# Performance work log

Measured on AMD Instinct MI355X. Metric: run time of the kernel, lower is better.

The kernel has to match this reference:

```python
import jax, jax.numpy as jnp
import numpy as np
from functools import partial

MASK_THRESH = 0.4
SCORE_THRESH = 0.35
SUPPRESS_IOU = 0.85
TOPK_KEEP = 40


def _logit(p):
    p = jnp.clip(p, 1e-4, 1.0 - 1e-4)
    return jnp.log(p) - jnp.log1p(-p)


def _greedy_keep(binm_f, labels, scores):
    # binm_f: [N, HW] float 0/1 masks, rows already sorted by descending score.
    # Precompute the pairwise mask-IoU matrix once (batched, memory-bound),
    # then run the sequential greedy suppression over the small NxN matrix.
    N = binm_f.shape[0]
    inter = binm_f @ binm_f.T                              # [N, N]
    area = jnp.sum(binm_f, axis=1)
    union = jnp.maximum(area[:, None] + area[None, :] - inter, 1.0)
    iou = inter / union
    conflict = (labels[:, None] == labels[None, :]) & (iou >= SUPPRESS_IOU)

    def body(i, state):
        kept, count, stopped = state
        stopped = stopped | (scores[i] < SCORE_THRESH)     # break on low score
        clash = jnp.any(kept & conflict[i])                # same-class high-IoU vs kept
        take = (~stopped) & (~clash)
        kept = kept.at[i].set(take)
        count = count + take.astype(jnp.int32)
        stopped = stopped | (count >= TOPK_KEEP)           # break after topk kept
        return kept, count, stopped

    kept0 = jnp.zeros((N,), dtype=bool)
    kept, count, _ = jax.lax.fori_loop(0, N, body, (kept0, jnp.int32(0), jnp.array(False)))
    return kept, count


def _per_image(masks, labels, scores, feat, class_count):
    N, H, W = masks.shape
    D, fh, fw = feat.shape
    order = jnp.argsort(-scores)
    masks = masks[order]
    labels = labels[order]
    scores = scores[order]
    binm = masks > MASK_THRESH
    kept, count = _greedy_keep(binm.reshape(N, -1).astype(masks.dtype), labels, scores)

    # pack kept entries into the leading slots, preserving score order
    key = jnp.where(kept, jnp.arange(N), N + jnp.arange(N))
    perm = jnp.argsort(key)
    masks_p = jnp.clip(masks[perm], 0.0, 1.0)
    labels_p = jnp.clip(labels[perm], 0, class_count - 1)
    scores_p = jnp.clip(scores[perm], 0.0, 1.0)
    valid = jnp.arange(N) < count                          # [Q], Q == N == max_queries

    mask_logits = jnp.where(valid[:, None, None], _logit(masks_p), -20.0)

    C1 = class_count + 1
    base = jnp.full((N, C1), -10.0, dtype=masks.dtype)     # default row (all -10)
    row = base.at[:, -1].set(0.0)                          # no-object col -> 0
    onehot = jax.nn.one_hot(labels_p, C1, dtype=masks.dtype)
    row = row + onehot * (_logit(scores_p)[:, None] + 10.0)
    class_logits = jnp.where(valid[:, None], row, base)

    binm_p = masks_p > MASK_THRESH
    xs = jnp.arange(W, dtype=masks.dtype)
    ys = jnp.arange(H, dtype=masks.dtype)
    big = jnp.asarray(1e9, masks.dtype)
    x1 = jnp.min(jnp.where(binm_p, xs[None, None, :], big), axis=(1, 2))
    x2 = jnp.max(jnp.where(binm_p, xs[None, None, :], -big), axis=(1, 2))
    y1 = jnp.min(jnp.where(binm_p, ys[None, :, None], big), axis=(1, 2))
    y2 = jnp.max(jnp.where(binm_p, ys[None, :, None], -big), axis=(1, 2))
    cx = (x1 + x2) * 0.5 / W
    cy = (y1 + y2) * 0.5 / H
    bw = jnp.maximum(x2 - x1, 0.0) / W
    bh = jnp.maximum(y2 - y1, 0.0) / H
    box = jnp.clip(jnp.stack([cx, cy, bw, bh], axis=-1), 0.0, 1.0)
    has_px = jnp.any(binm_p, axis=(1, 2))
    boxes = jnp.where((valid & has_px)[:, None], box, 0.0)

    # mask-pooled DINO embeddings (bilinear downsample == F.interpolate align_corners=False)
    mask_small = jax.image.resize(masks_p, (N, fh, fw), method='linear')
    denom = jnp.maximum(jnp.sum(mask_small, axis=(1, 2)), 1e-6)
    pooled = jnp.einsum('qhw,dhw->qd', mask_small, feat) / denom[:, None]
    norm = jnp.maximum(jnp.linalg.norm(pooled, axis=-1, keepdims=True), 1e-12)
    embs = jnp.where(valid[:, None], pooled / norm, 0.0)
    return mask_logits, class_logits, boxes, embs


def reference(masks, labels, scores, dino_feat_map, class_count):
    fn = lambda m, l, s, f: _per_image(m, l, s, f, class_count)
    return jax.vmap(fn)(masks, labels, scores, dino_feat_map)


def setup_inputs():
    key = jax.random.key(0)
    k1, k2, k3, k4 = jax.random.split(key, 4)
    B, N, H, W = 2, 100, 640, 640
    D, fh, fw = 384, 40, 40
    return {
        'masks': jax.random.uniform(k1, (B, N, H, W), dtype=jnp.float32),
        'labels': jax.random.randint(k2, (B, N), 0, 80),
        'scores': jax.random.uniform(k3, (B, N), dtype=jnp.float32),
        'dino_feat_map': jax.random.normal(k4, (B, D, fh, fw), dtype=jnp.float32),
        'class_count': 80,
    }
```

## Files before the change

### kernel.cpp

```cpp
#include <hip/hip_runtime.h>
#include <cstdint>
#include <climits>

constexpr int kB = 2;
constexpr int kN = 100;
constexpr int kH = 640;
constexpr int kW = 640;
constexpr int kHW = kH * kW;
constexpr int kWORDS = kHW / 64;
constexpr int kD = 384;
constexpr int kFH = 40;
constexpr int kFW = 40;
constexpr int kC = 80;
constexpr int kC1 = kC + 1;
constexpr int kTOPK = 40;
constexpr int kCW = 2;
constexpr int kPairMax = kN * (kN - 1) / 2;

constexpr float MASK_THRESH = 0.4f;
constexpr float SCORE_THRESH = 0.35f;
constexpr float SUPPRESS_IOU = 0.85f;

constexpr size_t O_MASK = 0;
constexpr size_t O_CLS  = (size_t)kB * kN * kHW;
constexpr size_t O_BOX  = O_CLS + (size_t)kB * kN * kC1;
constexpr size_t O_EMB  = O_BOX + (size_t)kB * kN * 4;

typedef float floatx4 __attribute__((ext_vector_type(4)));
__device__ __forceinline__ void nt_store4(const float4& v, float4* p) {
    floatx4 t; t.x = v.x; t.y = v.y; t.z = v.z; t.w = v.w;
    __builtin_nontemporal_store(t, (floatx4*)p);
}

__device__ __forceinline__ float logitf_(float p) {
    p = fminf(fmaxf(p, 1e-4f), 1.0f - 1e-4f);
    return logf(p) - log1pf(-p);
}

__device__ __forceinline__ float logit_fast(float p) {
    p = fminf(fmaxf(p, 1e-4f), 1.0f - 1e-4f);
    float r = __fdividef(p, 1.0f - p);
    return __log2f(r) * 0.69314718056f;
}

__global__ void k0_sort_init(const float* __restrict__ scores,
                             const int* __restrict__ labels,
                             int* __restrict__ order, float* __restrict__ sScore,
                             int* __restrict__ sLabel, int* __restrict__ area,
                             int* __restrict__ bbox,
                             unsigned long long* __restrict__ confRow,
                             float* __restrict__ denom,
                             int* __restrict__ pairList,
                             int* __restrict__ pairCount) {
    int b = blockIdx.x;
    int t = threadIdx.x;
    __shared__ float s[kN];
    __shared__ int   lb[kN];
    __shared__ float ssort[kN];
    __shared__ int   lsort[kN];
    if (t < kN) { s[t] = scores[b * kN + t]; lb[t] = labels[b * kN + t]; }
    if (t == 0) pairCount[b] = 0;
    __syncthreads();
    if (t < kN) {
        float si = s[t];
        int rank = 0;
        for (int j = 0; j < kN; ++j) {
            float sj = s[j];
            if (sj > si || (sj == si && j < t)) rank++;
        }
        order[b * kN + rank]  = t;
        sScore[b * kN + rank] = si;
        sLabel[b * kN + rank] = lb[t];
        ssort[rank] = si;
        lsort[rank] = lb[t];
        area[b * kN + t] = 0;
        bbox[(b * kN + t) * 4 + 0] = INT_MAX;
        bbox[(b * kN + t) * 4 + 1] = INT_MIN;
        bbox[(b * kN + t) * 4 + 2] = INT_MAX;
        bbox[(b * kN + t) * 4 + 3] = INT_MIN;
        confRow[(b * kN + t) * kCW + 0] = 0ull;
        confRow[(b * kN + t) * kCW + 1] = 0ull;
        if (t < kTOPK) denom[b * kTOPK + t] = 0.0f;
    }
    __syncthreads();
    for (int idx = t; idx < kN * kN; idx += 128) {
        int i = idx / kN, j = idx - i * kN;
        if (j < i && lsort[i] == lsort[j] && ssort[i] >= SCORE_THRESH) {
            int pos = atomicAdd(&pairCount[b], 1);
            pairList[b * kPairMax + pos] = (i << 16) | j;
        }
    }
}

constexpr int kSPLIT = 8;
__global__ __launch_bounds__(256) void k1_pack(
    const float* __restrict__ masks, const int* __restrict__ order,
    const float* __restrict__ sScore, unsigned long long* __restrict__ packed,
    int* __restrict__ area, int* __restrict__ bbox) {
    int b = blockIdx.z, slot = blockIdx.y;
    if (sScore[b * kN + slot] < SCORE_THRESH) return;
    int q = order[b * kN + slot];
    const float4* src = (const float4*)(masks + (size_t)(b * kN + q) * kHW);
    unsigned long long* dst = packed + (size_t)(b * kN + slot) * (size_t)kWORDS;
    int lane = threadIdx.x & 63;
    int wv = threadIdx.x >> 6;
    const int wordsPerBlock = kWORDS / kSPLIT;
    const int wordsPerWave = wordsPerBlock / 4;
    int wbase = blockIdx.x * wordsPerBlock + wv * wordsPerWave;
    int pixBase = wbase * 64;

    int areaAcc = 0;
    int x1 = INT_MAX, x2 = INT_MIN, y1 = INT_MAX, y2 = INT_MIN;
#pragma unroll 2
    for (int i = 0; i < wordsPerWave / 4; ++i) {
        int pix = pixBase + i * 256 + lane * 4;
        float4 v = src[pix >> 2];
        bool p0 = v.x > MASK_THRESH, p1 = v.y > MASK_THRESH;
        bool p2 = v.z > MASK_THRESH, p3 = v.w > MASK_THRESH;
        unsigned long long b0 = __ballot(p0);
        unsigned long long b1 = __ballot(p1);
        unsigned long long b2 = __ballot(p2);
        unsigned long long b3 = __ballot(p3);
        if (lane == 0) {
            dst[wbase + 4 * i + 0] = b0;
            dst[wbase + 4 * i + 1] = b1;
            dst[wbase + 4 * i + 2] = b2;
            dst[wbase + 4 * i + 3] = b3;
        }
        int cnt = (int)p0 + (int)p1 + (int)p2 + (int)p3;
        areaAcc += cnt;
        if (cnt) {
            int row  = pix / kW;
            int col0 = pix - row * kW;
            int lo = p0 ? 0 : (p1 ? 1 : (p2 ? 2 : 3));
            int hi = p3 ? 3 : (p2 ? 2 : (p1 ? 1 : 0));
            x1 = min(x1, col0 + lo); x2 = max(x2, col0 + hi);
            y1 = min(y1, row);       y2 = max(y2, row);
        }
    }
#pragma unroll
    for (int off = 32; off > 0; off >>= 1) {
        areaAcc += __shfl_down(areaAcc, off);
        x1 = min(x1, __shfl_down(x1, off));
        x2 = max(x2, __shfl_down(x2, off));
        y1 = min(y1, __shfl_down(y1, off));
        y2 = max(y2, __shfl_down(y2, off));
    }
    __shared__ int sA[4], sx1[4], sx2[4], sy1[4], sy2[4];
    if (lane == 0) { sA[wv] = areaAcc; sx1[wv] = x1; sx2[wv] = x2; sy1[wv] = y1; sy2[wv] = y2; }
    __syncthreads();
    if (threadIdx.x == 0) {
        int A   = sA[0] + sA[1] + sA[2] + sA[3];
        int bx1 = min(min(sx1[0], sx1[1]), min(sx1[2], sx1[3]));
        int bx2 = max(max(sx2[0], sx2[1]), max(sx2[2], sx2[3]));
        int by1 = min(min(sy1[0], sy1[1]), min(sy1[2], sy1[3]));
        int by2 = max(max(sy2[0], sy2[1]), max(sy2[2], sy2[3]));
        if (A) atomicAdd(&area[b * kN + slot], A);
        if (bx1 != INT_MAX) {
            atomicMin(&bbox[(b * kN + slot) * 4 + 0], bx1);
            atomicMax(&bbox[(b * kN + slot) * 4 + 1], bx2);
            atomicMin(&bbox[(b * kN + slot) * 4 + 2], by1);
            atomicMax(&bbox[(b * kN + slot) * 4 + 3], by2);
        }
    }
}

__global__ __launch_bounds__(256) void k2a_conflict(
    const unsigned long long* __restrict__ packed,
    const int* __restrict__ area, const int* __restrict__ pairList,
    const int* __restrict__ pairCount, unsigned long long* __restrict__ confRow) {
    int b = blockIdx.y;
    int np = pairCount[b];
    __shared__ int s[256];
    for (int p = blockIdx.x; p < np; p += gridDim.x) {
        int pr = pairList[b * kPairMax + p];
        int i = pr >> 16, j = pr & 0xffff;
        const unsigned long long* pi = packed + (size_t)(b * kN + i) * kWORDS;
        const unsigned long long* pj = packed + (size_t)(b * kN + j) * kWORDS;
        int acc = 0;
        for (int w = threadIdx.x; w < kWORDS; w += 256)
            acc += __popcll(pi[w] & pj[w]);
        s[threadIdx.x] = acc;
        __syncthreads();
        for (int st = 128; st > 0; st >>= 1) {
            if (threadIdx.x < st) s[threadIdx.x] += s[threadIdx.x + st];
            __syncthreads();
        }
        if (threadIdx.x == 0) {
            float inter = (float)s[0];
            float un = fmaxf((float)area[b * kN + i] + (float)area[b * kN + j] - inter, 1.0f);
            if (inter / un >= SUPPRESS_IOU)
                atomicOr(&confRow[(b * kN + i) * kCW + (j >> 6)], 1ull << (j & 63));
        }
        __syncthreads();
    }
}

__global__ __launch_bounds__(256) void k2b_greedy_clsbox(
    const float* __restrict__ sScore, const int* __restrict__ order,
    const unsigned long long* __restrict__ confRow,
    const int* __restrict__ sLabel, const int* __restrict__ area,
    const int* __restrict__ bbox, int* __restrict__ src_q,
    int* __restrict__ keep_s, int* __restrict__ countArr,
    float* __restrict__ out) {
    int b = blockIdx.x;
    int t = threadIdx.x;
    __shared__ float sc[kN];
    __shared__ int   ord[kN];
    __shared__ unsigned long long cr[kN * kCW];
    __shared__ int   ks[kN];
    __shared__ int   cnt_s;
    for (int e = t; e < kN; e += 256) {
        sc[e]  = sScore[b * kN + e];
        ord[e] = order[b * kN + e];
    }
    for (int e = t; e < kN * kCW; e += 256)
        cr[e] = confRow[(size_t)b * kN * kCW + e];
    __syncthreads();

    if (t == 0) {
        unsigned long long keptLo = 0ull, keptHi = 0ull;
        bool stopped = false;
        int count = 0;
        for (int i = 0; i < kN; ++i) {
            if (sc[i] < SCORE_THRESH) stopped = true;
            unsigned long long cl = cr[i * kCW + 0] & keptLo;
            unsigned long long ch = cr[i * kCW + 1] & keptHi;
            bool take = (!stopped) && ((cl | ch) == 0ull);
            if (take) {
                if (i < 64) keptLo |= 1ull << i; else keptHi |= 1ull << (i - 64);
                src_q[b * kN + count]  = ord[i];
                keep_s[b * kN + count] = i;
                ks[count] = i;
                count++;
                if (count >= kTOPK) stopped = true;
            }
        }
        countArr[b] = count;
        cnt_s = count;
        for (int s = count; s < kN; ++s) {
            src_q[b * kN + s] = -1; keep_s[b * kN + s] = -1; ks[s] = -1;
        }
    }
    __syncthreads();
    int count = cnt_s;

    for (int e = t; e < kN * kC1; e += 256) {
        int slot = e / kC1, c = e % kC1;
        float val = -10.0f;
        if (slot < count) {
            int s2 = ks[slot];
            int lab = min(max(sLabel[b * kN + s2], 0), kC - 1);
            float scv = fminf(fmaxf(sc[s2], 0.f), 1.f);
            if (c == lab) val = logitf_(scv);
            else if (c == kC1 - 1) val = 0.0f;
        }
        out[O_CLS + (size_t)b * kN * kC1 + e] = val;
    }
    for (int slot = t; slot < kN; slot += 256) {
        float bx[4] = {0.f, 0.f, 0.f, 0.f};
        if (slot < count) {
            int s2 = ks[slot];
            if (area[b * kN + s2] > 0) {
                float x1 = (float)bbox[(b * kN + s2) * 4 + 0];
                float x2 = (float)bbox[(b * kN + s2) * 4 + 1];
                float y1 = (float)bbox[(b * kN + s2) * 4 + 2];
                float y2 = (float)bbox[(b * kN + s2) * 4 + 3];
                bx[0] = fminf(fmaxf((x1 + x2) * 0.5f / kW, 0.f), 1.f);
                bx[1] = fminf(fmaxf((y1 + y2) * 0.5f / kH, 0.f), 1.f);
                bx[2] = fminf(fmaxf(fmaxf(x2 - x1, 0.f) / kW, 0.f), 1.f);
                bx[3] = fminf(fmaxf(fmaxf(y2 - y1, 0.f) / kH, 0.f), 1.f);
            }
        }
        for (int c4 = 0; c4 < 4; ++c4)
            out[O_BOX + (size_t)(b * kN + slot) * 4 + c4] = bx[c4];
    }
}

__global__ __launch_bounds__(256) void k3_logits_resizex(
    const float* __restrict__ masks, const int* __restrict__ src_q,
    float* __restrict__ out, float* __restrict__ S1) {
    int b = blockIdx.z, slot = blockIdx.y;
    int q = src_q[b * kN + slot];
    int lane = threadIdx.x & 63, wv = threadIdx.x >> 6;
    int y = blockIdx.x * 4 + wv;
    float4* dst = (float4*)(out + O_MASK + (size_t)(b * kN + slot) * kHW) + (size_t)y * 160;

    if (q < 0) {
        float4 f = make_float4(-20.f, -20.f, -20.f, -20.f);
        nt_store4(f, dst + lane);
        nt_store4(f, dst + 64 + lane);
        if (lane < 32) nt_store4(f, dst + 128 + lane);
        return;
    }

    __shared__ float rbuf[4][660];
    const float4* src = (const float4*)(masks + (size_t)(b * kN + q) * kHW) + (size_t)y * 160;
#pragma unroll
    for (int i = 0; i < 3; ++i) {
        int idx = i * 64 + lane;
        if (idx < 160) {
            float4 m = src[idx];
            float4 o;
            o.x = logit_fast(m.x); o.y = logit_fast(m.y);
            o.z = logit_fast(m.z); o.w = logit_fast(m.w);
            nt_store4(o, dst + idx);
            int col = idx * 4;
            int pad = col >> 5;
            rbuf[wv][col + pad + 0] = fminf(fmaxf(m.x, 0.f), 1.f);
            rbuf[wv][col + pad + 1] = fminf(fmaxf(m.y, 0.f), 1.f);
            rbuf[wv][col + pad + 2] = fminf(fmaxf(m.z, 0.f), 1.f);
            rbuf[wv][col + pad + 3] = fminf(fmaxf(m.w, 0.f), 1.f);
        }
    }
    __syncthreads();
    if (lane < kFW) {
        int ox = lane;
        float c = 16.0f * ox + 7.5f;
        float s = 0.f;
#pragma unroll
        for (int t = 0; t < 32; ++t) {
            int j = 16 * ox - 8 + t;
            if (j >= 0 && j < kW) {
                float w = 1.0f - fabsf((float)j - c) * (1.0f / 16.0f);
                s += w * rbuf[wv][j + (j >> 5)];
            }
        }
        float rs = (ox == 0 || ox == kFW - 1) ? (1.0f / 14.0f) : (1.0f / 16.0f);
        S1[((size_t)(b * kTOPK + slot) * kH + y) * kFW + ox] = s * rs;
    }
}

__global__ __launch_bounds__(256) void k3f_fill(float* __restrict__ out) {
    int b = blockIdx.y;
    float4* base = (float4*)(out + O_MASK + ((size_t)b * kN + kTOPK) * (size_t)kHW);
    const size_t n4 = (size_t)(kN - kTOPK) * kHW / 4;
    float4 f = make_float4(-20.f, -20.f, -20.f, -20.f);
    for (size_t i = (size_t)blockIdx.x * 256 + threadIdx.x; i < n4;
         i += (size_t)gridDim.x * 256)
        nt_store4(f, base + i);
}

__global__ __launch_bounds__(256) void k6_resize_y(
    const float* __restrict__ S1, const int* __restrict__ countArr,
    float* __restrict__ msmall, float* __restrict__ denom) {
    int k = blockIdx.y, b = blockIdx.z;
    if (k >= countArr[b]) return;
    const float* src = S1 + (size_t)(b * kTOPK + k) * kH * kFW;
    int e0 = blockIdx.x * 320;
    float tot = 0.f;
    for (int ee = threadIdx.x; ee < 320; ee += 256) {
        int e = e0 + ee;
        int oy = e / kFW, ox = e % kFW;
        float c = 16.0f * oy + 7.5f;
        int j0 = max(0, 16 * oy - 8), j1 = min(kH - 1, 16 * oy + 23);
        float s = 0.f;
        for (int j = j0; j <= j1; ++j) {
            float w = 1.0f - fabsf((float)j - c) * (1.0f / 16.0f);
            s += w * src[(size_t)j * kFW + ox];
        }
        float rs = (oy == 0 || oy == kFH - 1) ? (1.0f / 14.0f) : (1.0f / 16.0f);
        s *= rs;
        msmall[(size_t)(b * kTOPK + k) * kFH * kFW + e] = s;
        tot += s;
    }
    __shared__ float sm[256];
    sm[threadIdx.x] = tot;
    __syncthreads();
    for (int st = 128; st > 0; st >>= 1) {
        if (threadIdx.x < st) sm[threadIdx.x] += sm[threadIdx.x + st];
        __syncthreads();
    }
    if (threadIdx.x == 0) atomicAdd(&denom[b * kTOPK + k], sm[0]);
}

__global__ __launch_bounds__(256) void k7_pool(
    const float* __restrict__ feat, const float* __restrict__ msmall,
    const float* __restrict__ denom, const int* __restrict__ countArr,
    float* __restrict__ pooled) {
    int d = blockIdx.x, b = blockIdx.y;
    int lane = threadIdx.x & 63, wv = threadIdx.x >> 6;
    const float* fp = feat + ((size_t)b * kD + d) * (kFH * kFW);
    float f[25];
#pragma unroll
    for (int i = 0; i < 25; ++i) f[i] = fp[i * 64 + lane];
    int count = countArr[b];
    for (int k = wv; k < count; k += 4) {
        const float* sp = msmall + (size_t)(b * kTOPK + k) * (kFH * kFW);
        float acc = 0.f;
#pragma unroll
        for (int i = 0; i < 25; ++i) acc += f[i] * sp[i * 64 + lane];
        for (int off = 32; off > 0; off >>= 1) acc += __shfl_down(acc, off);
        if (lane == 0)
            pooled[(size_t)(b * kTOPK + k) * kD + d] =
                acc / fmaxf(denom[b * kTOPK + k], 1e-6f);
    }
}

__global__ void k8_embs(const float* __restrict__ pooled,
                        const int* __restrict__ countArr,
                        float* __restrict__ out) {
    int slot = blockIdx.x, b = blockIdx.y;
    int count = countArr[b];
    float* dst = out + O_EMB + (size_t)(b * kN + slot) * kD;
    if (slot >= count) {
        for (int e = threadIdx.x; e < kD; e += 128) dst[e] = 0.f;
        return;
    }
    const float* p = pooled + (size_t)(b * kTOPK + slot) * kD;
    float ss = 0.f;
    for (int e = threadIdx.x; e < kD; e += 128) { float v = p[e]; ss += v * v; }
    __shared__ float sm[128];
    sm[threadIdx.x] = ss;
    __syncthreads();
    for (int st = 64; st > 0; st >>= 1) {
        if (threadIdx.x < st) sm[threadIdx.x] += sm[threadIdx.x + st];
        __syncthreads();
    }
    float norm = fmaxf(sqrtf(sm[0]), 1e-12f);
    for (int e = threadIdx.x; e < kD; e += 128) dst[e] = p[e] / norm;
}

extern "C" void kernel_launch(void* const* d_in, const int* in_sizes, int n_in,
                              void* d_out, int out_size, void* d_ws, size_t ws_size,
                              hipStream_t stream) {
    const float* masks  = (const float*)d_in[0];
    const int*   labels = (const int*)d_in[1];
    const float* scores = (const float*)d_in[2];
    const float* feat   = (const float*)d_in[3];
    float* out = (float*)d_out;

    char* ws = (char*)d_ws;
    auto take = [&](size_t bytes) { char* p = ws; ws += (bytes + 255) & ~(size_t)255; return p; };
    unsigned long long* packed = (unsigned long long*)take((size_t)kB * kN * kWORDS * 8);
    float* S1     = (float*)take((size_t)kB * kTOPK * kH * kFW * 4);
    float* msmall = (float*)take((size_t)kB * kTOPK * kFH * kFW * 4);
    float* pooled = (float*)take((size_t)kB * kTOPK * kD * 4);
    float* sScore = (float*)take((size_t)kB * kN * 4);
    float* denom  = (float*)take((size_t)kB * kTOPK * 4);
    int* order    = (int*)take((size_t)kB * kN * 4);
    int* sLabel   = (int*)take((size_t)kB * kN * 4);
    int* area     = (int*)take((size_t)kB * kN * 4);
    int* bbox     = (int*)take((size_t)kB * kN * 4 * 4);
    int* src_q    = (int*)take((size_t)kB * kN * 4);
    int* keep_s   = (int*)take((size_t)kB * kN * 4);
    int* countArr = (int*)take((size_t)kB * 4);
    unsigned long long* confRow = (unsigned long long*)take((size_t)kB * kN * kCW * 8);
    int* pairList  = (int*)take((size_t)kB * kPairMax * 4);
    int* pairCount = (int*)take((size_t)kB * 4);

    k0_sort_init<<<dim3(kB), dim3(128), 0, stream>>>(scores, labels, order, sScore,
                                                     sLabel, area, bbox, confRow,
                                                     denom, pairList, pairCount);
    k1_pack<<<dim3(kSPLIT, kN, kB), dim3(256), 0, stream>>>(masks, order, sScore,
                                                            packed, area, bbox);
    k2a_conflict<<<dim3(512, kB), dim3(256), 0, stream>>>(packed, area, pairList,
                                                          pairCount, confRow);
    k2b_greedy_clsbox<<<dim3(kB), dim3(256), 0, stream>>>(sScore, order, confRow,
                                                          sLabel, area, bbox, src_q,
                                                          keep_s, countArr, out);
    k3_logits_resizex<<<dim3(kH / 4, kTOPK, kB), dim3(256), 0, stream>>>(masks, src_q,
                                                                         out, S1);
    k3f_fill<<<dim3(1024, kB), dim3(256), 0, stream>>>(out);
    k6_resize_y<<<dim3(5, kTOPK, kB), dim3(256), 0, stream>>>(S1, countArr, msmall,
                                                              denom);
    k7_pool<<<dim3(kD, kB), dim3(256), 0, stream>>>(feat, msmall, denom, countArr,
                                                    pooled);
    k8_embs<<<dim3(kN, kB), dim3(128), 0, stream>>>(pooled, countArr, out);
}
```

Measured before the change: 628.9 us.

## Fuse sort, conflict, greedy NMS and pooling kernels to cut launches and atomics

Removes the separate init kernel by having each pack block recompute the score rank itself and write per-split partial area and bbox values instead of atomics. The pairwise conflict computation, greedy suppression and class/box output are merged into one 1024-thread block per image, using wave-level reductions and shared-memory conflict bits. The y-resize, pooling and normalisation stages are fused into one kernel per kept slot, and the fill kernel is moved first. Fewer launches and less global round-tripping, at the cost of running the conflict popcounts on only two blocks, which lowers parallelism for that step.

Result: slower. 702.8 us (+11.8%).

```diff
diff --git a/kernel.cpp b/kernel.cpp
--- a/kernel.cpp
+++ b/kernel.cpp
@@ -14,7 +14,6 @@
 constexpr int kC = 80;
 constexpr int kC1 = kC + 1;
 constexpr int kTOPK = 40;
-constexpr int kCW = 2;
 constexpr int kPairMax = kN * (kN - 1) / 2;
 
 constexpr float MASK_THRESH = 0.4f;
@@ -43,67 +42,45 @@
     return __log2f(r) * 0.69314718056f;
 }
 
-__global__ void k0_sort_init(const float* __restrict__ scores,
-                             const int* __restrict__ labels,
-                             int* __restrict__ order, float* __restrict__ sScore,
-                             int* __restrict__ sLabel, int* __restrict__ area,
-                             int* __restrict__ bbox,
-                             unsigned long long* __restrict__ confRow,
-                             float* __restrict__ denom,
-                             int* __restrict__ pairList,
-                             int* __restrict__ pairCount) {
-    int b = blockIdx.x;
+__global__ __launch_bounds__(256) void k3f_fill(float* __restrict__ out) {
+    int b = blockIdx.y;
+    float4* base = (float4*)(out + O_MASK + ((size_t)b * kN + kTOPK) * (size_t)kHW);
+    const size_t n4 = (size_t)(kN - kTOPK) * kHW / 4;
+    float4 f = make_float4(-20.f, -20.f, -20.f, -20.f);
+    for (size_t i = (size_t)blockIdx.x * 256 + threadIdx.x; i < n4;
+         i += (size_t)gridDim.x * 256)
+        nt_store4(f, base + i);
+}
+
+constexpr int kSPLIT = 8;
+__global__ __launch_bounds__(256) void k1_pack(
+    const float* __restrict__ masks, const float* __restrict__ scores,
+    unsigned long long* __restrict__ packed, int* __restrict__ areaPart,
+    int* __restrict__ bboxPart) {
+    int b = blockIdx.z, slot = blockIdx.y;
     int t = threadIdx.x;
-    __shared__ float s[kN];
-    __shared__ int   lb[kN];
-    __shared__ float ssort[kN];
-    __shared__ int   lsort[kN];
-    if (t < kN) { s[t] = scores[b * kN + t]; lb[t] = labels[b * kN + t]; }
-    if (t == 0) pairCount[b] = 0;
+    __shared__ float sS[kN];
+    __shared__ int sQ;
+    __shared__ float sSc;
+    if (t < kN) sS[t] = scores[b * kN + t];
     __syncthreads();
     if (t < kN) {
-        float si = s[t];
+        float si = sS[t];
         int rank = 0;
         for (int j = 0; j < kN; ++j) {
-            float sj = s[j];
+            float sj = sS[j];
             if (sj > si || (sj == si && j < t)) rank++;
         }
-        order[b * kN + rank]  = t;
-        sScore[b * kN + rank] = si;
-        sLabel[b * kN + rank] = lb[t];
-        ssort[rank] = si;
-        lsort[rank] = lb[t];
-        area[b * kN + t] = 0;
-        bbox[(b * kN + t) * 4 + 0] = INT_MAX;
-        bbox[(b * kN + t) * 4 + 1] = INT_MIN;
-        bbox[(b * kN + t) * 4 + 2] = INT_MAX;
-        bbox[(b * kN + t) * 4 + 3] = INT_MIN;
-        confRow[(b * kN + t) * kCW + 0] = 0ull;
-        confRow[(b * kN + t) * kCW + 1] = 0ull;
-        if (t < kTOPK) denom[b * kTOPK + t] = 0.0f;
-    }
-    __syncthreads();
-    for (int idx = t; idx < kN * kN; idx += 128) {
-        int i = idx / kN, j = idx - i * kN;
-        if (j < i && lsort[i] == lsort[j] && ssort[i] >= SCORE_THRESH) {
-            int pos = atomicAdd(&pairCount[b], 1);
-            pairList[b * kPairMax + pos] = (i << 16) | j;
-        }
-    }
-}
-
-constexpr int kSPLIT = 8;
-__global__ __launch_bounds__(256) void k1_pack(
-    const float* __restrict__ masks, const int* __restrict__ order,
-    const float* __restrict__ sScore, unsigned long long* __restrict__ packed,
-    int* __restrict__ area, int* __restrict__ bbox) {
-    int b = blockIdx.z, slot = blockIdx.y;
-    if (sScore[b * kN + slot] < SCORE_THRESH) return;
-    int q = order[b * kN + slot];
+        if (rank == slot) { sQ = t; sSc = si; }
+    }
+    __syncthreads();
+    if (sSc < SCORE_THRESH) return;
+    int q = sQ;
+
     const float4* src = (const float4*)(masks + (size_t)(b * kN + q) * kHW);
     unsigned long long* dst = packed + (size_t)(b * kN + slot) * (size_t)kWORDS;
-    int lane = threadIdx.x & 63;
-    int wv = threadIdx.x >> 6;
+    int lane = t & 63;
+    int wv = t >> 6;
     const int wordsPerBlock = kWORDS / kSPLIT;
     const int wordsPerWave = wordsPerBlock / 4;
     int wbase = blockIdx.x * wordsPerBlock + wv * wordsPerWave;
@@ -149,127 +126,140 @@
     __shared__ int sA[4], sx1[4], sx2[4], sy1[4], sy2[4];
     if (lane == 0) { sA[wv] = areaAcc; sx1[wv] = x1; sx2[wv] = x2; sy1[wv] = y1; sy2[wv] = y2; }
     __syncthreads();
-    if (threadIdx.x == 0) {
+    if (t == 0) {
         int A   = sA[0] + sA[1] + sA[2] + sA[3];
         int bx1 = min(min(sx1[0], sx1[1]), min(sx1[2], sx1[3]));
         int bx2 = max(max(sx2[0], sx2[1]), max(sx2[2], sx2[3]));
         int by1 = min(min(sy1[0], sy1[1]), min(sy1[2], sy1[3]));
         int by2 = max(max(sy2[0], sy2[1]), max(sy2[2], sy2[3]));
-        if (A) atomicAdd(&area[b * kN + slot], A);
-        if (bx1 != INT_MAX) {
-            atomicMin(&bbox[(b * kN + slot) * 4 + 0], bx1);
-            atomicMax(&bbox[(b * kN + slot) * 4 + 1], bx2);
-            atomicMin(&bbox[(b * kN + slot) * 4 + 2], by1);
-            atomicMax(&bbox[(b * kN + slot) * 4 + 3], by2);
-        }
-    }
-}
-
-__global__ __launch_bounds__(256) void k2a_conflict(
+        areaPart[(b * kN + slot) * kSPLIT + blockIdx.x] = A;
+        int* bp = bboxPart + ((b * kN + slot) * kSPLIT + blockIdx.x) * 4;
+        bp[0] = bx1; bp[1] = bx2; bp[2] = by1; bp[3] = by2;
+    }
+}
+
+__global__ __launch_bounds__(1024) void k2_nms_clsbox(
+    const float* __restrict__ scores, const int* __restrict__ labels,
     const unsigned long long* __restrict__ packed,
-    const int* __restrict__ area, const int* __restrict__ pairList,
-    const int* __restrict__ pairCount, unsigned long long* __restrict__ confRow) {
-    int b = blockIdx.y;
-    int np = pairCount[b];
-    __shared__ int s[256];
-    for (int p = blockIdx.x; p < np; p += gridDim.x) {
-        int pr = pairList[b * kPairMax + p];
+    const int* __restrict__ areaPart, const int* __restrict__ bboxPart,
+    int* __restrict__ src_q, int* __restrict__ countArr,
+    float* __restrict__ out) {
+    int b = blockIdx.x;
+    int t = threadIdx.x;
+    __shared__ float sRaw[kN];
+    __shared__ int   lRaw[kN];
+    __shared__ float ssort[kN];
+    __shared__ int   lsort[kN];
+    __shared__ int   ordL[kN];
+    __shared__ int   areaS[kN];
+    __shared__ unsigned int conf[kN][4];
+    __shared__ int   pairL[kPairMax];
+    __shared__ int   pairN;
+    __shared__ int   ksL[kN];
+    __shared__ int   cntS;
+
+    if (t < kN) { sRaw[t] = scores[b * kN + t]; lRaw[t] = labels[b * kN + t]; }
+    if (t == 0) pairN = 0;
+    for (int e = t; e < kN * 4; e += 1024) conf[e >> 2][e & 3] = 0u;
+    __syncthreads();
+    if (t < kN) {
+        float si = sRaw[t];
+        int rank = 0;
+        for (int j = 0; j < kN; ++j) {
+            float sj = sRaw[j];
+            if (sj > si || (sj == si && j < t)) rank++;
+        }
+        ssort[rank] = si; lsort[rank] = lRaw[t]; ordL[rank] = t;
+    }
+    __syncthreads();
+    if (t < kN) {
+        int a = 0;
+        if (ssort[t] >= SCORE_THRESH)
+            for (int p = 0; p < kSPLIT; ++p) a += areaPart[(b * kN + t) * kSPLIT + p];
+        areaS[t] = a;
+    }
+    for (int idx = t; idx < kN * kN; idx += 1024) {
+        int i = idx / kN, j = idx - i * kN;
+        if (j < i && lsort[i] == lsort[j] && ssort[i] >= SCORE_THRESH) {
+            int pos = atomicAdd(&pairN, 1);
+            pairL[pos] = (i << 16) | j;
+        }
+    }
+    __syncthreads();
+    int lane = t & 63, wv = t >> 6;
+    int np = pairN;
+    for (int p = wv; p < np; p += 16) {
+        int pr = pairL[p];
         int i = pr >> 16, j = pr & 0xffff;
         const unsigned long long* pi = packed + (size_t)(b * kN + i) * kWORDS;
         const unsigned long long* pj = packed + (size_t)(b * kN + j) * kWORDS;
         int acc = 0;
-        for (int w = threadIdx.x; w < kWORDS; w += 256)
+        for (int w = lane; w < kWORDS; w += 64)
             acc += __popcll(pi[w] & pj[w]);
-        s[threadIdx.x] = acc;
-        __syncthreads();
-        for (int st = 128; st > 0; st >>= 1) {
-            if (threadIdx.x < st) s[threadIdx.x] += s[threadIdx.x + st];
-            __syncthreads();
-        }
-        if (threadIdx.x == 0) {
-            float inter = (float)s[0];
-            float un = fmaxf((float)area[b * kN + i] + (float)area[b * kN + j] - inter, 1.0f);
+#pragma unroll
+        for (int off = 32; off > 0; off >>= 1) acc += __shfl_down(acc, off);
+        if (lane == 0) {
+            float inter = (float)acc;
+            float un = fmaxf((float)areaS[i] + (float)areaS[j] - inter, 1.0f);
             if (inter / un >= SUPPRESS_IOU)
-                atomicOr(&confRow[(b * kN + i) * kCW + (j >> 6)], 1ull << (j & 63));
-        }
-        __syncthreads();
-    }
-}
-
-__global__ __launch_bounds__(256) void k2b_greedy_clsbox(
-    const float* __restrict__ sScore, const int* __restrict__ order,
-    const unsigned long long* __restrict__ confRow,
-    const int* __restrict__ sLabel, const int* __restrict__ area,
-    const int* __restrict__ bbox, int* __restrict__ src_q,
-    int* __restrict__ keep_s, int* __restrict__ countArr,
-    float* __restrict__ out) {
-    int b = blockIdx.x;
-    int t = threadIdx.x;
-    __shared__ float sc[kN];
-    __shared__ int   ord[kN];
-    __shared__ unsigned long long cr[kN * kCW];
-    __shared__ int   ks[kN];
-    __shared__ int   cnt_s;
-    for (int e = t; e < kN; e += 256) {
-        sc[e]  = sScore[b * kN + e];
-        ord[e] = order[b * kN + e];
-    }
-    for (int e = t; e < kN * kCW; e += 256)
-        cr[e] = confRow[(size_t)b * kN * kCW + e];
-    __syncthreads();
-
+                atomicOr(&conf[i][j >> 5], 1u << (j & 31));
+        }
+    }
+    __syncthreads();
     if (t == 0) {
-        unsigned long long keptLo = 0ull, keptHi = 0ull;
+        unsigned int kept[4] = {0u, 0u, 0u, 0u};
         bool stopped = false;
         int count = 0;
         for (int i = 0; i < kN; ++i) {
-            if (sc[i] < SCORE_THRESH) stopped = true;
-            unsigned long long cl = cr[i * kCW + 0] & keptLo;
-            unsigned long long ch = cr[i * kCW + 1] & keptHi;
-            bool take = (!stopped) && ((cl | ch) == 0ull);
+            if (ssort[i] < SCORE_THRESH) stopped = true;
+            unsigned int cl = (conf[i][0] & kept[0]) | (conf[i][1] & kept[1]) |
+                              (conf[i][2] & kept[2]) | (conf[i][3] & kept[3]);
+            bool take = (!stopped) && (cl == 0u);
             if (take) {
-                if (i < 64) keptLo |= 1ull << i; else keptHi |= 1ull << (i - 64);
-                src_q[b * kN + count]  = ord[i];
-                keep_s[b * kN + count] = i;
-                ks[count] = i;
+                kept[i >> 5] |= 1u << (i & 31);
+                src_q[b * kN + count] = ordL[i];
+                ksL[count] = i;
                 count++;
                 if (count >= kTOPK) stopped = true;
             }
         }
         countArr[b] = count;
-        cnt_s = count;
-        for (int s = count; s < kN; ++s) {
-            src_q[b * kN + s] = -1; keep_s[b * kN + s] = -1; ks[s] = -1;
-        }
-    }
-    __syncthreads();
-    int count = cnt_s;
-
-    for (int e = t; e < kN * kC1; e += 256) {
-        int slot = e / kC1, c = e % kC1;
+        cntS = count;
+        for (int s = count; s < kN; ++s) { src_q[b * kN + s] = -1; ksL[s] = -1; }
+    }
+    __syncthreads();
+    int count = cntS;
+
+    for (int e = t; e < kN * kC1; e += 1024) {
+        int slot = e / kC1, c = e - slot * kC1;
         float val = -10.0f;
         if (slot < count) {
-            int s2 = ks[slot];
-            int lab = min(max(sLabel[b * kN + s2], 0), kC - 1);
-            float scv = fminf(fmaxf(sc[s2], 0.f), 1.f);
+            int s2 = ksL[slot];
+            int lab = min(max(lsort[s2], 0), kC - 1);
+            float scv = fminf(fmaxf(ssort[s2], 0.f), 1.f);
             if (c == lab) val = logitf_(scv);
             else if (c == kC1 - 1) val = 0.0f;
         }
         out[O_CLS + (size_t)b * kN * kC1 + e] = val;
     }
-    for (int slot = t; slot < kN; slot += 256) {
+    if (t < kN) {
+        int slot = t;
         float bx[4] = {0.f, 0.f, 0.f, 0.f};
         if (slot < count) {
-            int s2 = ks[slot];
-            if (area[b * kN + s2] > 0) {
-                float x1 = (float)bbox[(b * kN + s2) * 4 + 0];
-                float x2 = (float)bbox[(b * kN + s2) * 4 + 1];
-                float y1 = (float)bbox[(b * kN + s2) * 4 + 2];
-                float y2 = (float)bbox[(b * kN + s2) * 4 + 3];
-                bx[0] = fminf(fmaxf((x1 + x2) * 0.5f / kW, 0.f), 1.f);
-                bx[1] = fminf(fmaxf((y1 + y2) * 0.5f / kH, 0.f), 1.f);
-                bx[2] = fminf(fmaxf(fmaxf(x2 - x1, 0.f) / kW, 0.f), 1.f);
-                bx[3] = fminf(fmaxf(fmaxf(y2 - y1, 0.f) / kH, 0.f), 1.f);
+            int s2 = ksL[slot];
+            if (areaS[s2] > 0) {
+                int x1 = INT_MAX, x2 = INT_MIN, y1 = INT_MAX, y2 = INT_MIN;
+                for (int p = 0; p < kSPLIT; ++p) {
+                    const int* bp = bboxPart + ((b * kN + s2) * kSPLIT + p) * 4;
+                    x1 = min(x1, bp[0]); x2 = max(x2, bp[1]);
+                    y1 = min(y1, bp[2]); y2 = max(y2, bp[3]);
+                }
+                float fx1 = (float)x1, fx2 = (float)x2;
+                float fy1 = (float)y1, fy2 = (float)y2;
+                bx[0] = fminf(fmaxf((fx1 + fx2) * 0.5f / kW, 0.f), 1.f);
+                bx[1] = fminf(fmaxf((fy1 + fy2) * 0.5f / kH, 0.f), 1.f);
+                bx[2] = fminf(fmaxf(fmaxf(fx2 - fx1, 0.f) / kW, 0.f), 1.f);
+                bx[3] = fminf(fmaxf(fmaxf(fy2 - fy1, 0.f) / kH, 0.f), 1.f);
             }
         }
         for (int c4 = 0; c4 < 4; ++c4)
@@ -319,8 +309,8 @@
         float c = 16.0f * ox + 7.5f;
         float s = 0.f;
 #pragma unroll
-        for (int t = 0; t < 32; ++t) {
-            int j = 16 * ox - 8 + t;
+        for (int tap = 0; tap < 32; ++tap) {
+            int j = 16 * ox - 8 + tap;
             if (j >= 0 && j < kW) {
                 float w = 1.0f - fabsf((float)j - c) * (1.0f / 16.0f);
                 s += w * rbuf[wv][j + (j >> 5)];
@@ -331,94 +321,65 @@
     }
 }
 
-__global__ __launch_bounds__(256) void k3f_fill(float* __restrict__ out) {
-    int b = blockIdx.y;
-    float4* base = (float4*)(out + O_MASK + ((size_t)b * kN + kTOPK) * (size_t)kHW);
-    const size_t n4 = (size_t)(kN - kTOPK) * kHW / 4;
-    float4 f = make_float4(-20.f, -20.f, -20.f, -20.f);
-    for (size_t i = (size_t)blockIdx.x * 256 + threadIdx.x; i < n4;
-         i += (size_t)gridDim.x * 256)
-        nt_store4(f, base + i);
-}
-
-__global__ __launch_bounds__(256) void k6_resize_y(
-    const float* __restrict__ S1, const int* __restrict__ countArr,
-    float* __restrict__ msmall, float* __restrict__ denom) {
-    int k = blockIdx.y, b = blockIdx.z;
-    if (k >= countArr[b]) return;
-    const float* src = S1 + (size_t)(b * kTOPK + k) * kH * kFW;
-    int e0 = blockIdx.x * 320;
+__global__ __launch_bounds__(512) void k9_pool_embs(
+    const float* __restrict__ S1, const float* __restrict__ feat,
+    const int* __restrict__ countArr, float* __restrict__ out) {
+    int slot = blockIdx.x, b = blockIdx.y;
+    int t = threadIdx.x;
+    int count = countArr[b];
+    float* dst = out + O_EMB + (size_t)(b * kN + slot) * kD;
+    if (slot >= count) {
+        if (t < kD) dst[t] = 0.f;
+        return;
+    }
+    __shared__ float ms[kFH * kFW];
+    __shared__ float pld[kD];
+    __shared__ float red[512];
+    const float* src = S1 + (size_t)(b * kTOPK + slot) * kH * kFW;
     float tot = 0.f;
-    for (int ee = threadIdx.x; ee < 320; ee += 256) {
-        int e = e0 + ee;
-        int oy = e / kFW, ox = e % kFW;
+    for (int e = t; e < kFH * kFW; e += 512) {
+        int oy = e / kFW, ox = e - oy * kFW;
         float c = 16.0f * oy + 7.5f;
         int j0 = max(0, 16 * oy - 8), j1 = min(kH - 1, 16 * oy + 23);
         float s = 0.f;
         for (int j = j0; j <= j1; ++j) {
             float w = 1.0f - fabsf((float)j - c) * (1.0f / 16.0f);
-            s += w * src[(size_t)j * kFW + ox];
+            s += w * src[j * kFW + ox];
         }
         float rs = (oy == 0 || oy == kFH - 1) ? (1.0f / 14.0f) : (1.0f / 16.0f);
         s *= rs;
-        msmall[(size_t)(b * kTOPK + k) * kFH * kFW + e] = s;
+        ms[e] = s;
         tot += s;
     }
-    __shared__ float sm[256];
-    sm[threadIdx.x] = tot;
-    __syncthreads();
-    for (int st = 128; st > 0; st >>= 1) {
-        if (threadIdx.x < st) sm[threadIdx.x] += sm[threadIdx.x + st];
+    red[t] = tot;
+    __syncthreads();
+    for (int st = 256; st > 0; st >>= 1) {
+        if (t < st) red[t] += red[t + st];
         __syncthreads();
     }
-    if (threadIdx.x == 0) atomicAdd(&denom[b * kTOPK + k], sm[0]);
-}
-
-__global__ __launch_bounds__(256) void k7_pool(
-    const float* __restrict__ feat, const float* __restrict__ msmall,
-    const float* __restrict__ denom, const int* __restrict__ countArr,
-    float* __restrict__ pooled) {
-    int d = blockIdx.x, b = blockIdx.y;
-    int lane = threadIdx.x & 63, wv = threadIdx.x >> 6;
-    const float* fp = feat + ((size_t)b * kD + d) * (kFH * kFW);
-    float f[25];
-#pragma unroll
-    for (int i = 0; i < 25; ++i) f[i] = fp[i * 64 + lane];
-    int count = countArr[b];
-    for (int k = wv; k < count; k += 4) {
-        const float* sp = msmall + (size_t)(b * kTOPK + k) * (kFH * kFW);
+    float denomC = fmaxf(red[0], 1e-6f);
+
+    int lane = t & 63, wv = t >> 6;
+    for (int d = wv; d < kD; d += 8) {
+        const float* fp = feat + ((size_t)b * kD + d) * (kFH * kFW);
         float acc = 0.f;
 #pragma unroll
-        for (int i = 0; i < 25; ++i) acc += f[i] * sp[i * 64 + lane];
+        for (int r = 0; r < 25; ++r) acc += fp[r * 64 + lane] * ms[r * 64 + lane];
+#pragma unroll
         for (int off = 32; off > 0; off >>= 1) acc += __shfl_down(acc, off);
-        if (lane == 0)
-            pooled[(size_t)(b * kTOPK + k) * kD + d] =
-                acc / fmaxf(denom[b * kTOPK + k], 1e-6f);
-    }
-}
-
-__global__ void k8_embs(const float* __restrict__ pooled,
-                        const int* __restrict__ countArr,
-                        float* __restrict__ out) {
-    int slot = blockIdx.x, b = blockIdx.y;
-    int count = countArr[b];
-    float* dst = out + O_EMB + (size_t)(b * kN + slot) * kD;
-    if (slot >= count) {
-        for (int e = threadIdx.x; e < kD; e += 128) dst[e] = 0.f;
-        return;
-    }
-    const float* p = pooled + (size_t)(b * kTOPK + slot) * kD;
+        if (lane == 0) pld[d] = acc / denomC;
+    }
+    __syncthreads();
     float ss = 0.f;
-    for (int e = threadIdx.x; e < kD; e += 128) { float v = p[e]; ss += v * v; }
-    __shared__ float sm[128];
-    sm[threadIdx.x] = ss;
-    __syncthreads();
-    for (int st = 64; st > 0; st >>= 1) {
-        if (threadIdx.x < st) sm[threadIdx.x] += sm[threadIdx.x + st];
+    if (t < kD) { float v = pld[t]; ss = v * v; }
+    red[t] = ss;
+    __syncthreads();
+    for (int st = 256; st > 0; st >>= 1) {
+        if (t < st) red[t] += red[t + st];
         __syncthreads();
     }
-    float norm = fmaxf(sqrtf(sm[0]), 1e-12f);
-    for (int e = threadIdx.x; e < kD; e += 128) dst[e] = p[e] / norm;
+    float norm = fmaxf(sqrtf(red[0]), 1e-12f);
+    if (t < kD) dst[t] = pld[t] / norm;
 }
 
 extern "C" void kernel_launch(void* const* d_in, const int* in_sizes, int n_in,
@@ -433,38 +394,19 @@
     char* ws = (char*)d_ws;
     auto take = [&](size_t bytes) { char* p = ws; ws += (bytes + 255) & ~(size_t)255; return p; };
     unsigned long long* packed = (unsigned long long*)take((size_t)kB * kN * kWORDS * 8);
-    float* S1     = (float*)take((size_t)kB * kTOPK * kH * kFW * 4);
-    float* msmall = (float*)take((size_t)kB * kTOPK * kFH * kFW * 4);
-    float* pooled = (float*)take((size_t)kB * kTOPK * kD * 4);
-    float* sScore = (float*)take((size_t)kB * kN * 4);
-    float* denom  = (float*)take((size_t)kB * kTOPK * 4);
-    int* order    = (int*)take((size_t)kB * kN * 4);
-    int* sLabel   = (int*)take((size_t)kB * kN * 4);
-    int* area     = (int*)take((size_t)kB * kN * 4);
-    int* bbox     = (int*)take((size_t)kB * kN * 4 * 4);
-    int* src_q    = (int*)take((size_t)kB * kN * 4);
-    int* keep_s   = (int*)take((size_t)kB * kN * 4);
-    int* countArr = (int*)take((size_t)kB * 4);
-    unsigned long long* confRow = (unsigned long long*)take((size_t)kB * kN * kCW * 8);
-    int* pairList  = (int*)take((size_t)kB * kPairMax * 4);
-    int* pairCount = (int*)take((size_t)kB * 4);
-
-    k0_sort_init<<<dim3(kB), dim3(128), 0, stream>>>(scores, labels, order, sScore,
-                                                     sLabel, area, bbox, confRow,
-                                                     denom, pairList, pairCount);
-    k1_pack<<<dim3(kSPLIT, kN, kB), dim3(256), 0, stream>>>(masks, order, sScore,
-                                                            packed, area, bbox);
-    k2a_conflict<<<dim3(512, kB), dim3(256), 0, stream>>>(packed, area, pairList,
-                                                          pairCount, confRow);
-    k2b_greedy_clsbox<<<dim3(kB), dim3(256), 0, stream>>>(sScore, order, confRow,
-                                                          sLabel, area, bbox, src_q,
-                                                          keep_s, countArr, out);
+    float* S1      = (float*)take((size_t)kB * kTOPK * kH * kFW * 4);
+    int* areaPart  = (int*)take((size_t)kB * kN * kSPLIT * 4);
+    int* bboxPart  = (int*)take((size_t)kB * kN * kSPLIT * 4 * 4);
+    int* src_q     = (int*)take((size_t)kB * kN * 4);
+    int* countArr  = (int*)take((size_t)kB * 4);
+
+    k3f_fill<<<dim3(1024, kB), dim3(256), 0, stream>>>(out);
+    k1_pack<<<dim3(kSPLIT, kN, kB), dim3(256), 0, stream>>>(masks, scores, packed,
+                                                            areaPart, bboxPart);
+    k2_nms_clsbox<<<dim3(kB), dim3(1024), 0, stream>>>(scores, labels, packed,
+                                                       areaPart, bboxPart, src_q,
+                                                       countArr, out);
     k3_logits_resizex<<<dim3(kH / 4, kTOPK, kB), dim3(256), 0, stream>>>(masks, src_q,
                                                                          out, S1);
-    k3f_fill<<<dim3(1024, kB), dim3(256), 0, stream>>>(out);
-    k6_resize_y<<<dim3(5, kTOPK, kB), dim3(256), 0, stream>>>(S1, countArr, msmall,
-                                                              denom);
-    k7_pool<<<dim3(kD, kB), dim3(256), 0, stream>>>(feat, msmall, denom, countArr,
-                                                    pooled);
-    k8_embs<<<dim3(kN, kB), dim3(128), 0, stream>>>(pooled, countArr, out);
-}
+    k9_pool_embs<<<dim3(kN, kB), dim3(512), 0, stream>>>(S1, feat, countArr, out);
+}
```
